# Performance work log

Hardware: AMD Instinct MI355X
Metric: run time of the kernel (lower is better)

Reference implementation:

```python
import jax, jax.numpy as jnp
import numpy as np

N = 30000        # nodes
E = 150000       # edges
IN = 16          # in_feats
H = 32           # hidden_feats
C = 10           # num_classes


def setup_inputs() -> dict:
    key = jax.random.key(0)
    ks = jax.random.split(key, 11)
    s = 0.05
    return {
        "x": jax.random.normal(ks[0], (N, IN), jnp.float32),
        "edge_attr": jax.random.normal(ks[1], (E, 1), jnp.float32),
        "W1": jax.random.normal(ks[2], (1, IN * H), jnp.float32) * s,
        "b1": jax.random.normal(ks[3], (IN * H,), jnp.float32) * s,
        "W2": jax.random.normal(ks[4], (IN * H, IN * H), jnp.float32) * s,
        "b2": jax.random.normal(ks[5], (IN * H,), jnp.float32) * s,
        "root": jax.random.normal(ks[6], (IN, H), jnp.float32) * s,
        "bias1": jax.random.normal(ks[7], (H,), jnp.float32) * s,
        "Wg": jax.random.normal(ks[8], (H, C), jnp.float32) * s,
        "bg": jax.random.normal(ks[9], (C,), jnp.float32) * s,
        "edge_index": jax.random.randint(ks[10], (2, E), 0, N),
    }


def _forward(x, edge_attr, W1, b1, W2, b2, root, bias1, Wg, bg, edge_index):
    src, dst = edge_index[0], edge_index[1]

    # ---- NNConv: edge-MLP generates per-edge [IN, H] weight matrices ----
    h = jax.nn.relu(edge_attr @ W1 + b1)          # [E, IN*H]
    theta = (h @ W2 + b2).reshape(E, IN, H)       # [E, IN, H]
    msg = jnp.einsum('ei,eio->eo', x[src], theta)  # per-edge matvec [E, H]
    summed = jax.ops.segment_sum(msg, dst, num_segments=N)            # [N, H]
    cnt = jax.ops.segment_sum(jnp.ones((E,), x.dtype), dst, num_segments=N)
    aggr = summed / jnp.maximum(cnt, 1.0)[:, None]  # mean aggregation
    h1 = aggr + x @ root + bias1                    # root weight + bias
    h1 = jax.nn.relu(h1)
    # dropout skipped (eval mode)

    # ---- GCNConv with self-loops and symmetric normalization ----
    xw = h1 @ Wg                                   # [N, C]
    loop = jnp.arange(N)
    row = jnp.concatenate([src, loop])
    col = jnp.concatenate([dst, loop])
    deg = jax.ops.segment_sum(jnp.ones(row.shape, x.dtype), col, num_segments=N)
    dinv = jnp.where(deg > 0, jax.lax.rsqrt(jnp.maximum(deg, 1e-12)), 0.0)
    norm = dinv[row] * dinv[col]                   # [E+N]
    out = jax.ops.segment_sum(xw[row] * norm[:, None], col, num_segments=N) + bg

    return jax.nn.log_softmax(out, axis=1)


def reference(x, edge_attr, W1, b1, W2, b2, root, bias1, Wg, bg, edge_index):
    return _forward(x, edge_attr, W1, b1, W2, b2, root, bias1, Wg, bg, edge_index)
```

## Files before the change

kernel.cpp:

```cpp
#include <hip/hip_runtime.h>
#include <math.h>

#define N_NODES 30000
#define N_EDGES 150000
#define NB_E ((N_EDGES + 255) / 256)

__device__ __forceinline__ unsigned bf16_rne(float f) {
    unsigned u = __float_as_uint(f);
    u += 0x7FFFu + ((u >> 16) & 1u);
    return u >> 16;
}

__global__ void k1z_rank(const float* __restrict__ W1, const float* __restrict__ b1,
                         float* __restrict__ tsort, int* __restrict__ ksort,
                         int* __restrict__ zbase ) {
    if (blockIdx.x == 0) {
        __shared__ float st[512];
        int tid = threadIdx.x;
        float w = W1[tid], b = b1[tid];
        float t = (w != 0.0f) ? (-b / w) : 3.0e38f;
        st[tid] = t;
        __syncthreads();
        int rank = 0;
#pragma unroll 8
        for (int j = 0; j < 512; ++j) {
            float tj = st[j];
            rank += (tj < t || (tj == t && j < tid)) ? 1 : 0;
        }
        tsort[rank] = t;
        ksort[rank] = tid;
    } else {
        int4* dz = (int4*)zbase;
        const int n4 = N_NODES * 33 / 4;
        int4 z = make_int4(0, 0, 0, 0);
        for (int i = (blockIdx.x - 1) * 512 + threadIdx.x; i < n4; i += 31 * 512)
            dz[i] = z;
    }
}

__global__ void __launch_bounds__(256) f2_prep(
        const int* __restrict__ ei, const float* __restrict__ ea,
        const float* __restrict__ tsort,
        int* __restrict__ deg, int* __restrict__ rankm,
        const float* __restrict__ W1, const float* __restrict__ b1,
        const float* __restrict__ W2, const int* __restrict__ ksort,
        float* __restrict__ PbA, float* __restrict__ PbB,
        float* __restrict__ SA, float* __restrict__ SB) {
    if (blockIdx.x < NB_E) {
        __shared__ float ts[512];
        for (int i = threadIdx.x; i < 512; i += 256) ts[i] = tsort[i];
        __syncthreads();
        int e = blockIdx.x * 256 + threadIdx.x;
        if (e >= N_EDGES) return;
        int rank = atomicAdd(&deg[ei[N_EDGES + e]], 1);
        float a = ea[e];
        int lo = 0, hi = 512;
        while (lo < hi) {
            int mid = (lo + hi) >> 1;
            if (ts[mid] < a) lo = mid + 1; else hi = mid;
        }
        rankm[e] = (rank << 10) | lo;
    } else {
        int bb = blockIdx.x - NB_E;
        int c = bb & 31;
        int jc = bb >> 5;
        int jt = jc * 256 + threadIdx.x;
        int jsrc = ((jt & 15) << 5) | (jt >> 4);
        float ba = 0.0f, bb2 = 0.0f, sa = 0.0f, sb = 0.0f;
#pragma unroll 4
        for (int s = 0; s < 16; ++s) {
            int k = c * 16 + s;
            float w = W1[k], b = b1[k];
            bool act = (w < 0.0f) || (w == 0.0f && b > 0.0f);
            if (act) {
                float w2 = W2[k * 512 + jsrc];
                ba = fmaf(w, w2, ba);
                bb2 = fmaf(b, w2, bb2);
            }
            int kr = ksort[c * 16 + s];
            float wr = W1[kr], br = b1[kr];
            float sgn = (wr > 0.0f) ? 1.0f : ((wr < 0.0f) ? -1.0f : 0.0f);
            float w2r = W2[kr * 512 + jsrc];
            sa = fmaf(sgn * wr, w2r, sa);
            sb = fmaf(sgn * br, w2r, sb);
        }
        PbA[c * 512 + jt] = ba; PbB[c * 512 + jt] = bb2;
        SA[c * 512 + jt] = sa;  SB[c * 512 + jt] = sb;
    }
}

__global__ void __launch_bounds__(1024) f3_scan_emit(
        const int* __restrict__ deg, int* __restrict__ offs,
        const float* __restrict__ W1, const float* __restrict__ b1,
        const float* __restrict__ b2, const float* __restrict__ W2,
        const int* __restrict__ ksort,
        const float* __restrict__ PbA, const float* __restrict__ PbB,
        const float* __restrict__ SA, const float* __restrict__ SB,
        unsigned int* __restrict__ T) {
    __shared__ int part[1024];
    if (blockIdx.x == 0) {
        int t = threadIdx.x;
        int base = t * 30;
        int loc[30];
        int s = 0;
#pragma unroll
        for (int i = 0; i < 30; ++i) {
            int idx = base + i;
            int v = (idx < N_NODES) ? deg[idx] : 0;
            loc[i] = v;
            s += v;
        }
        part[t] = s;
        __syncthreads();
        for (int off = 1; off < 1024; off <<= 1) {
            int v = part[t];
            int add = (t >= off) ? part[t - off] : 0;
            __syncthreads();
            part[t] = v + add;
            __syncthreads();
        }
        int run = (t > 0) ? part[t - 1] : 0;
#pragma unroll
        for (int i = 0; i < 30; ++i) {
            int idx = base + i;
            if (idx < N_NODES) offs[idx] = run;
            run += loc[i];
        }
        if (t == 1023) offs[N_NODES] = run;
    } else {
        int c = (blockIdx.x - 1) * 2 + (threadIdx.x >> 9);
        int jt = threadIdx.x & 511;
        int jsrc = ((jt & 15) << 5) | (jt >> 4);
        float runA = 0.0f, runB = 0.0f;
#pragma unroll
        for (int c2 = 0; c2 < 32; ++c2) {
            runA += PbA[c2 * 512 + jt];
            runB += PbB[c2 * 512 + jt];
            if (c2 < c) { runA += SA[c2 * 512 + jt]; runB += SB[c2 * 512 + jt]; }
        }
        float bb2 = b2[jsrc];
#pragma unroll 4
        for (int s = 0; s < 16; ++s) {
            int m = c * 16 + s;
            T[m * 512 + jt] = (bf16_rne(runA) << 16) | bf16_rne(runB + bb2);
            int k = ksort[m];
            float w = W1[k], b = b1[k];
            float sgn = (w > 0.0f) ? 1.0f : ((w < 0.0f) ? -1.0f : 0.0f);
            float w2 = W2[k * 512 + jsrc];
            runA = fmaf(sgn * w, w2, runA);
            runB = fmaf(sgn * b, w2, runB);
        }
        if (c == 31) {
            T[512 * 512 + jt] = (bf16_rne(runA) << 16) | bf16_rne(runB + bb2);
        }
    }
}

__global__ void __launch_bounds__(256) k3_edges(
        const float* __restrict__ x, const float* __restrict__ ea,
        const int* __restrict__ ei, const int* __restrict__ rankm,
        const int* __restrict__ offs, const unsigned int* __restrict__ T,
        float* __restrict__ summed, int* __restrict__ ssrc) {
    int gid = blockIdx.x * blockDim.x + threadIdx.x;
    int lane = gid & 31;
    int g = gid >> 5;
    int e0 = g << 1;
    if (e0 >= N_EDGES) return;
    float2 aa = *(const float2*)(ea + e0);
    int2 ss = *(const int2*)(ei + e0);
    int2 dd = *(const int2*)(ei + N_EDGES + e0);
    int2 rr = *(const int2*)(rankm + e0);
    int m0 = rr.x & 1023, m1 = rr.y & 1023;
    const uint4* T0 = (const uint4*)(T + m0 * 512 + lane * 16);
    const uint4* T1 = (const uint4*)(T + m1 * 512 + lane * 16);
    uint4 p0 = T0[0], p1 = T0[1], p2 = T0[2], p3 = T0[3];
    uint4 q0 = T1[0], q1 = T1[1], q2 = T1[2], q3 = T1[3];
    float xv0 = (lane < 16) ? x[ss.x * 16 + lane] : 0.0f;
    float xv1 = (lane < 16) ? x[ss.y * 16 + lane] : 0.0f;
    float xa0 = 0.0f, xb0 = 0.0f, xa1 = 0.0f, xb1 = 0.0f;
    float xi;
#define STEP2(w0, w1, i)                                                   \
    xi = __shfl(xv0, i, 32);                                               \
    xa0 = fmaf(xi, __uint_as_float((w0) & 0xFFFF0000u), xa0);              \
    xb0 = fmaf(xi, __uint_as_float((w0) << 16), xb0);                      \
    xi = __shfl(xv1, i, 32);                                               \
    xa1 = fmaf(xi, __uint_as_float((w1) & 0xFFFF0000u), xa1);              \
    xb1 = fmaf(xi, __uint_as_float((w1) << 16), xb1);
    STEP2(p0.x, q0.x, 0)  STEP2(p0.y, q0.y, 1)  STEP2(p0.z, q0.z, 2)  STEP2(p0.w, q0.w, 3)
    STEP2(p1.x, q1.x, 4)  STEP2(p1.y, q1.y, 5)  STEP2(p1.z, q1.z, 6)  STEP2(p1.w, q1.w, 7)
    STEP2(p2.x, q2.x, 8)  STEP2(p2.y, q2.y, 9)  STEP2(p2.z, q2.z, 10) STEP2(p2.w, q2.w, 11)
    STEP2(p3.x, q3.x, 12) STEP2(p3.y, q3.y, 13) STEP2(p3.z, q3.z, 14) STEP2(p3.w, q3.w, 15)
#undef STEP2
    float msg0 = fmaf(aa.x, xa0, xb0);
    float msg1 = fmaf(aa.y, xa1, xb1);
    atomicAdd(&summed[dd.x * 32 + lane], msg0);
    atomicAdd(&summed[dd.y * 32 + lane], msg1);
    if (lane == 0) {
        ssrc[offs[dd.x] + (rr.x >> 10)] = ss.x;
        ssrc[offs[dd.y] + (rr.y >> 10)] = ss.y;
    }
}

__global__ void k4_nodes(const float* __restrict__ x, const int* __restrict__ offs,
                         const float* __restrict__ summed,
                         const float* __restrict__ root, const float* __restrict__ bias1,
                         const float* __restrict__ Wg,
                         float* __restrict__ xw12) {
    __shared__ float sroot[512], sb1[32], swg[320];
    for (int i = threadIdx.x; i < 512; i += blockDim.x) sroot[i] = root[i];
    for (int i = threadIdx.x; i < 32; i += blockDim.x) sb1[i] = bias1[i];
    for (int i = threadIdx.x; i < 320; i += blockDim.x) swg[i] = Wg[i];
    __syncthreads();
    int n = blockIdx.x * blockDim.x + threadIdx.x;
    if (n >= N_NODES) return;
    float c = (float)(offs[n + 1] - offs[n]);
    float inv = 1.0f / fmaxf(c, 1.0f);
    const float4* xp = (const float4*)(x + n * 16);
    float xr[16];
#pragma unroll
    for (int q = 0; q < 4; ++q) {
        float4 v = xp[q];
        xr[q * 4 + 0] = v.x; xr[q * 4 + 1] = v.y;
        xr[q * 4 + 2] = v.z; xr[q * 4 + 3] = v.w;
    }
    const float4* sp = (const float4*)(summed + n * 32);
    float sm[32];
#pragma unroll
    for (int q = 0; q < 8; ++q) {
        float4 v = sp[q];
        sm[q * 4 + 0] = v.x; sm[q * 4 + 1] = v.y;
        sm[q * 4 + 2] = v.z; sm[q * 4 + 3] = v.w;
    }
    float acc[10];
#pragma unroll
    for (int cc = 0; cc < 10; ++cc) acc[cc] = 0.0f;
#pragma unroll
    for (int o = 0; o < 32; ++o) {
        float h = sm[o] * inv + sb1[o];
#pragma unroll
        for (int i = 0; i < 16; ++i) h = fmaf(xr[i], sroot[i * 32 + o], h);
        h = fmaxf(h, 0.0f);
#pragma unroll
        for (int cc = 0; cc < 10; ++cc) acc[cc] = fmaf(h, swg[o * 10 + cc], acc[cc]);
    }
    float4* op = (float4*)(xw12 + n * 12);
    op[0] = make_float4(acc[0], acc[1], acc[2], acc[3]);
    op[1] = make_float4(acc[4], acc[5], acc[6], acc[7]);
    op[2] = make_float4(acc[8], acc[9], rsqrtf(c + 1.0f), 0.0f);
}

__global__ void k56_final(const int* __restrict__ offs, const int* __restrict__ ssrc,
                          const float* __restrict__ xw12,
                          const float* __restrict__ bg, float* __restrict__ out) {
    __shared__ float sbg[16];
    if (threadIdx.x < 10) sbg[threadIdx.x] = bg[threadIdx.x];
    __syncthreads();
    int n = blockIdx.x * blockDim.x + threadIdx.x;
    if (n >= N_NODES) return;
    const float4* base = (const float4*)xw12;
    float4 r0 = base[n * 3], r1 = base[n * 3 + 1], r2 = base[n * 3 + 2];
    float dn = r2.z;
    float d2 = dn * dn;
    float acc[10];
    acc[0] = fmaf(r0.x, d2, sbg[0]); acc[1] = fmaf(r0.y, d2, sbg[1]);
    acc[2] = fmaf(r0.z, d2, sbg[2]); acc[3] = fmaf(r0.w, d2, sbg[3]);
    acc[4] = fmaf(r1.x, d2, sbg[4]); acc[5] = fmaf(r1.y, d2, sbg[5]);
    acc[6] = fmaf(r1.z, d2, sbg[6]); acc[7] = fmaf(r1.w, d2, sbg[7]);
    acc[8] = fmaf(r2.x, d2, sbg[8]); acc[9] = fmaf(r2.y, d2, sbg[9]);
    int s0 = offs[n], s1 = offs[n + 1];
    for (int sl = s0; sl < s1; ++sl) {
        int s = ssrc[sl];
        float4 q0 = base[s * 3], q1 = base[s * 3 + 1], q2 = base[s * 3 + 2];
        float nf = q2.z * dn;
        acc[0] = fmaf(q0.x, nf, acc[0]); acc[1] = fmaf(q0.y, nf, acc[1]);
        acc[2] = fmaf(q0.z, nf, acc[2]); acc[3] = fmaf(q0.w, nf, acc[3]);
        acc[4] = fmaf(q1.x, nf, acc[4]); acc[5] = fmaf(q1.y, nf, acc[5]);
        acc[6] = fmaf(q1.z, nf, acc[6]); acc[7] = fmaf(q1.w, nf, acc[7]);
        acc[8] = fmaf(q2.x, nf, acc[8]); acc[9] = fmaf(q2.y, nf, acc[9]);
    }
    float mx = -1e30f;
#pragma unroll
    for (int c = 0; c < 10; ++c) mx = fmaxf(mx, acc[c]);
    float se = 0.0f;
#pragma unroll
    for (int c = 0; c < 10; ++c) se += expf(acc[c] - mx);
    float lse = logf(se) + mx;
#pragma unroll
    for (int c = 0; c < 10; ++c) out[n * 10 + c] = acc[c] - lse;
}

extern "C" void kernel_launch(void* const* d_in, const int* in_sizes, int n_in,
                              void* d_out, int out_size, void* d_ws, size_t ws_size,
                              hipStream_t stream) {
    const float* x     = (const float*)d_in[0];
    const float* ea    = (const float*)d_in[1];
    const float* W1    = (const float*)d_in[2];
    const float* b1    = (const float*)d_in[3];
    const float* W2    = (const float*)d_in[4];
    const float* b2    = (const float*)d_in[5];
    const float* root  = (const float*)d_in[6];
    const float* bias1 = (const float*)d_in[7];
    const float* Wg    = (const float*)d_in[8];
    const float* bg    = (const float*)d_in[9];
    const int*   ei    = (const int*)d_in[10];
    float* out = (float*)d_out;

    unsigned int* T = (unsigned int*)d_ws;
    float* tsort  = (float*)(T + 513 * 512);
    int*   ksort  = (int*)(tsort + 512);
    float* summed = (float*)(ksort + 512);
    int*   deg    = (int*)(summed + N_NODES * 32);
    int*   offs   = deg + N_NODES;
    int*   rankm  = offs + N_NODES + 4;
    int*   ssrc   = rankm + N_EDGES;
    float* xw12   = (float*)(ssrc + N_EDGES);
    float* PbA    = xw12 + N_NODES * 12;
    float* PbB    = PbA + 32 * 512;
    float* SA     = PbB + 32 * 512;
    float* SB     = SA + 32 * 512;

    k1z_rank<<<32, 512, 0, stream>>>(W1, b1, tsort, ksort, (int*)summed);
    f2_prep<<<NB_E + 64, 256, 0, stream>>>(ei, ea, tsort, deg, rankm,
                                           W1, b1, W2, ksort, PbA, PbB, SA, SB);
    f3_scan_emit<<<17, 1024, 0, stream>>>(deg, offs, W1, b1, b2, W2, ksort,
                                          PbA, PbB, SA, SB, T);
    k3_edges<<<(N_EDGES / 2 * 32 + 255) / 256, 256, 0, stream>>>(
        x, ea, ei, rankm, offs, T, summed, ssrc);
    k4_nodes<<<(N_NODES + 255) / 256, 256, 0, stream>>>(x, offs, summed,
                                                        root, bias1, Wg, xw12);
    k56_final<<<(N_NODES + 255) / 256, 256, 0, stream>>>(offs, ssrc, xw12, bg, out);
}
```

Baseline: 105.3 us.

## Build bf16 lookup table in single pass inside edge-prep kernel

Replaces the chunked partial-sum computation of the piecewise-linear lookup table with a direct sequential accumulation over all 512 hidden units per output column, done inside the edge-prep kernel using shared-memory copies of W1, b1 and the sort order. The degree scan becomes its own single-block kernel, and the zeroing grid is widened. This removes the intermediate partial buffers and the combine step, but serialises about a thousand dependent W2 loads per thread on just two blocks.

Result: slower. 261.6 us (+148.6%).

```diff
diff --git a/kernel.cpp b/kernel.cpp
--- a/kernel.cpp
+++ b/kernel.cpp
@@ -33,7 +33,7 @@
         int4* dz = (int4*)zbase;
         const int n4 = N_NODES * 33 / 4;
         int4 z = make_int4(0, 0, 0, 0);
-        for (int i = (blockIdx.x - 1) * 512 + threadIdx.x; i < n4; i += 31 * 512)
+        for (int i = (blockIdx.x - 1) * 512 + threadIdx.x; i < n4; i += 255 * 512)
             dz[i] = z;
     }
 }
@@ -43,12 +43,11 @@
         const float* __restrict__ tsort,
         int* __restrict__ deg, int* __restrict__ rankm,
         const float* __restrict__ W1, const float* __restrict__ b1,
-        const float* __restrict__ W2, const int* __restrict__ ksort,
-        float* __restrict__ PbA, float* __restrict__ PbB,
-        float* __restrict__ SA, float* __restrict__ SB) {
+        const float* __restrict__ b2, const float* __restrict__ W2,
+        const int* __restrict__ ksort, unsigned int* __restrict__ T) {
+    __shared__ float sh[1536];
     if (blockIdx.x < NB_E) {
-        __shared__ float ts[512];
-        for (int i = threadIdx.x; i < 512; i += 256) ts[i] = tsort[i];
+        for (int i = threadIdx.x; i < 512; i += 256) sh[i] = tsort[i];
         __syncthreads();
         int e = blockIdx.x * 256 + threadIdx.x;
         if (e >= N_EDGES) return;
@@ -57,103 +56,76 @@
         int lo = 0, hi = 512;
         while (lo < hi) {
             int mid = (lo + hi) >> 1;
-            if (ts[mid] < a) lo = mid + 1; else hi = mid;
+            if (sh[mid] < a) lo = mid + 1; else hi = mid;
         }
         rankm[e] = (rank << 10) | lo;
     } else {
-        int bb = blockIdx.x - NB_E;
-        int c = bb & 31;
-        int jc = bb >> 5;
-        int jt = jc * 256 + threadIdx.x;
+        int* ks = (int*)(sh + 1024);
+        for (int i = threadIdx.x; i < 512; i += 256) {
+            sh[i] = W1[i];
+            sh[512 + i] = b1[i];
+            ks[i] = ksort[i];
+        }
+        __syncthreads();
+        int jt = (blockIdx.x - NB_E) * 256 + threadIdx.x;
         int jsrc = ((jt & 15) << 5) | (jt >> 4);
-        float ba = 0.0f, bb2 = 0.0f, sa = 0.0f, sb = 0.0f;
+        float runA = 0.0f, runB = 0.0f;
 #pragma unroll 4
-        for (int s = 0; s < 16; ++s) {
-            int k = c * 16 + s;
-            float w = W1[k], b = b1[k];
+        for (int k = 0; k < 512; ++k) {
+            float w = sh[k], b = sh[512 + k];
             bool act = (w < 0.0f) || (w == 0.0f && b > 0.0f);
             if (act) {
                 float w2 = W2[k * 512 + jsrc];
-                ba = fmaf(w, w2, ba);
-                bb2 = fmaf(b, w2, bb2);
+                runA = fmaf(w, w2, runA);
+                runB = fmaf(b, w2, runB);
             }
-            int kr = ksort[c * 16 + s];
-            float wr = W1[kr], br = b1[kr];
-            float sgn = (wr > 0.0f) ? 1.0f : ((wr < 0.0f) ? -1.0f : 0.0f);
-            float w2r = W2[kr * 512 + jsrc];
-            sa = fmaf(sgn * wr, w2r, sa);
-            sb = fmaf(sgn * br, w2r, sb);
-        }
-        PbA[c * 512 + jt] = ba; PbB[c * 512 + jt] = bb2;
-        SA[c * 512 + jt] = sa;  SB[c * 512 + jt] = sb;
-    }
-}
-
-__global__ void __launch_bounds__(1024) f3_scan_emit(
-        const int* __restrict__ deg, int* __restrict__ offs,
-        const float* __restrict__ W1, const float* __restrict__ b1,
-        const float* __restrict__ b2, const float* __restrict__ W2,
-        const int* __restrict__ ksort,
-        const float* __restrict__ PbA, const float* __restrict__ PbB,
-        const float* __restrict__ SA, const float* __restrict__ SB,
-        unsigned int* __restrict__ T) {
-    __shared__ int part[1024];
-    if (blockIdx.x == 0) {
-        int t = threadIdx.x;
-        int base = t * 30;
-        int loc[30];
-        int s = 0;
-#pragma unroll
-        for (int i = 0; i < 30; ++i) {
-            int idx = base + i;
-            int v = (idx < N_NODES) ? deg[idx] : 0;
-            loc[i] = v;
-            s += v;
-        }
-        part[t] = s;
-        __syncthreads();
-        for (int off = 1; off < 1024; off <<= 1) {
-            int v = part[t];
-            int add = (t >= off) ? part[t - off] : 0;
-            __syncthreads();
-            part[t] = v + add;
-            __syncthreads();
-        }
-        int run = (t > 0) ? part[t - 1] : 0;
-#pragma unroll
-        for (int i = 0; i < 30; ++i) {
-            int idx = base + i;
-            if (idx < N_NODES) offs[idx] = run;
-            run += loc[i];
-        }
-        if (t == 1023) offs[N_NODES] = run;
-    } else {
-        int c = (blockIdx.x - 1) * 2 + (threadIdx.x >> 9);
-        int jt = threadIdx.x & 511;
-        int jsrc = ((jt & 15) << 5) | (jt >> 4);
-        float runA = 0.0f, runB = 0.0f;
-#pragma unroll
-        for (int c2 = 0; c2 < 32; ++c2) {
-            runA += PbA[c2 * 512 + jt];
-            runB += PbB[c2 * 512 + jt];
-            if (c2 < c) { runA += SA[c2 * 512 + jt]; runB += SB[c2 * 512 + jt]; }
         }
         float bb2 = b2[jsrc];
 #pragma unroll 4
-        for (int s = 0; s < 16; ++s) {
-            int m = c * 16 + s;
-            T[m * 512 + jt] = (bf16_rne(runA) << 16) | bf16_rne(runB + bb2);
-            int k = ksort[m];
-            float w = W1[k], b = b1[k];
+        for (int r = 0; r < 512; ++r) {
+            T[r * 512 + jt] = (bf16_rne(runA) << 16) | bf16_rne(runB + bb2);
+            int k = ks[r];
+            float w = sh[k], b = sh[512 + k];
             float sgn = (w > 0.0f) ? 1.0f : ((w < 0.0f) ? -1.0f : 0.0f);
             float w2 = W2[k * 512 + jsrc];
             runA = fmaf(sgn * w, w2, runA);
             runB = fmaf(sgn * b, w2, runB);
         }
-        if (c == 31) {
-            T[512 * 512 + jt] = (bf16_rne(runA) << 16) | bf16_rne(runB + bb2);
-        }
-    }
+        T[512 * 512 + jt] = (bf16_rne(runA) << 16) | bf16_rne(runB + bb2);
+    }
+}
+
+__global__ void __launch_bounds__(1024) f3_scan(
+        const int* __restrict__ deg, int* __restrict__ offs) {
+    __shared__ int part[1024];
+    int t = threadIdx.x;
+    int base = t * 30;
+    int loc[30];
+    int s = 0;
+#pragma unroll
+    for (int i = 0; i < 30; ++i) {
+        int idx = base + i;
+        int v = (idx < N_NODES) ? deg[idx] : 0;
+        loc[i] = v;
+        s += v;
+    }
+    part[t] = s;
+    __syncthreads();
+    for (int off = 1; off < 1024; off <<= 1) {
+        int v = part[t];
+        int add = (t >= off) ? part[t - off] : 0;
+        __syncthreads();
+        part[t] = v + add;
+        __syncthreads();
+    }
+    int run = (t > 0) ? part[t - 1] : 0;
+#pragma unroll
+    for (int i = 0; i < 30; ++i) {
+        int idx = base + i;
+        if (idx < N_NODES) offs[idx] = run;
+        run += loc[i];
+    }
+    if (t == 1023) offs[N_NODES] = run;
 }
 
 __global__ void __launch_bounds__(256) k3_edges(
@@ -314,16 +286,11 @@
     int*   rankm  = offs + N_NODES + 4;
     int*   ssrc   = rankm + N_EDGES;
     float* xw12   = (float*)(ssrc + N_EDGES);
-    float* PbA    = xw12 + N_NODES * 12;
-    float* PbB    = PbA + 32 * 512;
-    float* SA     = PbB + 32 * 512;
-    float* SB     = SA + 32 * 512;
-
-    k1z_rank<<<32, 512, 0, stream>>>(W1, b1, tsort, ksort, (int*)summed);
-    f2_prep<<<NB_E + 64, 256, 0, stream>>>(ei, ea, tsort, deg, rankm,
-                                           W1, b1, W2, ksort, PbA, PbB, SA, SB);
-    f3_scan_emit<<<17, 1024, 0, stream>>>(deg, offs, W1, b1, b2, W2, ksort,
-                                          PbA, PbB, SA, SB, T);
+
+    k1z_rank<<<256, 512, 0, stream>>>(W1, b1, tsort, ksort, (int*)summed);
+    f2_prep<<<NB_E + 2, 256, 0, stream>>>(ei, ea, tsort, deg, rankm,
+                                          W1, b1, b2, W2, ksort, T);
+    f3_scan<<<1, 1024, 0, stream>>>(deg, offs);
     k3_edges<<<(N_EDGES / 2 * 32 + 255) / 256, 256, 0, stream>>>(
         x, ea, ei, rankm, offs, T, summed, ssrc);
     k4_nodes<<<(N_NODES + 255) / 256, 256, 0, stream>>>(x, offs, summed,
```
